# Kernel tuning notes

Hardware: AMD Instinct MI355X
Metric: run time of the kernel (lower is better)

## Reference

```python
import jax, jax.numpy as jnp
import numpy as np
from jax import lax

WIN = 7
K1 = 0.01
K2 = 0.03


def _box(t, w):
    # 'valid' box filter: uniform WINxWIN window, matches F.conv2d(t, w)
    return lax.conv_general_dilated(
        t, w, window_strides=(1, 1), padding='VALID',
        dimension_numbers=('NCHW', 'OIHW', 'NCHW'))


def setup_inputs() -> dict:
    key = jax.random.key(0)
    kx, ky = jax.random.split(key)
    X = jax.random.uniform(kx, (256, 1, 320, 320), dtype=jnp.float32)
    Y = jax.random.uniform(ky, (256, 1, 320, 320), dtype=jnp.float32)
    return {"X": X, "Y": Y}


def reference(X, Y):
    NP = WIN * WIN
    cov_norm = NP / (NP - 1)  # unbiased covariance correction
    w = jnp.ones((1, 1, WIN, WIN), X.dtype) / NP

    # per-sample dynamic range of the reference image Y -> [B,1,1,1]
    data_range = jnp.max(Y, axis=(1, 2, 3), keepdims=True)
    C1 = (K1 * data_range) ** 2
    C2 = (K2 * data_range) ** 2

    ux = _box(X, w)
    uy = _box(Y, w)
    uxx = _box(X * X, w)
    uyy = _box(Y * Y, w)
    uxy = _box(X * Y, w)

    vx = cov_norm * (uxx - ux * ux)
    vy = cov_norm * (uyy - uy * uy)
    vxy = cov_norm * (uxy - ux * uy)

    A1 = 2 * ux * uy + C1
    A2 = 2 * vxy + C2
    B1 = ux * ux + uy * uy + C1
    B2 = vx + vy + C2

    S = (A1 * A2) / (B1 * B2)
    S = jnp.mean(S)          # reduced=True
    return 1.0 - S           # as_loss=True
```

## Files before the change

### kernel.cpp

```cpp
#include <hip/hip_runtime.h>

#define BATCH 256
#define IMH 320
#define IMW 320
#define OUTD 314
#define WIN7 7
#define TOX 122
#define RCH 80

__global__ __launch_bounds__(256) void k_max(const float* __restrict__ Y,
                                             unsigned* __restrict__ dr) {
    int bid = blockIdx.x;
    int b = bid >> 2, part = bid & 3;
    const float4* p = (const float4*)(Y + (size_t)b * (IMH * IMW) + part * (IMH * IMW / 4));
    float m = 0.f;
    for (int i = threadIdx.x; i < (IMH * IMW / 16); i += 256) {
        float4 v = p[i];
        m = fmaxf(m, fmaxf(fmaxf(v.x, v.y), fmaxf(v.z, v.w)));
    }
    for (int off = 32; off; off >>= 1) m = fmaxf(m, __shfl_down(m, off, 64));
    __shared__ float sm[4];
    int lane = threadIdx.x & 63, wv = threadIdx.x >> 6;
    if (lane == 0) sm[wv] = m;
    __syncthreads();
    if (threadIdx.x == 0) {
        m = fmaxf(fmaxf(sm[0], sm[1]), fmaxf(sm[2], sm[3]));
        atomicMax(dr + b, __float_as_uint(m));
    }
}

__global__ __launch_bounds__(128) void k_ssim(const float* __restrict__ X,
                                              const float* __restrict__ Y,
                                              const unsigned* __restrict__ dr,
                                              double* __restrict__ acc) {
    int idx = blockIdx.x;
    int b = idx / 12;
    int rem = idx - b * 12;
    int ct = rem % 3;
    int rc = rem / 3;
    int t  = threadIdx.x;
    int c  = ct * TOX + t;
    int r0 = rc * RCH;
    int nout = min(RCH, OUTD - r0);
    bool colload = (c < IMW);

    const size_t base = (size_t)b * (IMH * IMW);
    const float* Xp = X + base;
    const float* Yp = Y + base;

    float drv = __uint_as_float(dr[b]);
    float c1r = 0.01f * drv, c2r = 0.03f * drv;
    float C1 = c1r * c1r;
    float C2 = c2r * c2r;

    __shared__ float vs[5][132];

    float x0=0,x1=0,x2=0,x3=0,x4=0,x5=0,x6=0;
    float y0=0,y1=0,y2=0,y3=0,y4=0,y5=0,y6=0;
    float sx=0, sy=0, sxx=0, syy=0, sxy=0;
    float part = 0.f;

    int rend = r0 + nout + (WIN7 - 2);
    for (int r = r0; r <= rend; ++r) {
        float xn = 0.f, yn = 0.f;
        if (colload) {
            xn = Xp[(size_t)r * IMW + c];
            yn = Yp[(size_t)r * IMW + c];
        }
        sx  += xn - x0;
        sy  += yn - y0;
        sxx += xn * xn - x0 * x0;
        syy += yn * yn - y0 * y0;
        sxy += xn * yn - x0 * y0;
        x0=x1; x1=x2; x2=x3; x3=x4; x4=x5; x5=x6; x6=xn;
        y0=y1; y1=y2; y2=y3; y3=y4; y4=y5; y5=y6; y6=yn;

        if (r - r0 >= WIN7 - 1) {
            vs[0][t]=sx; vs[1][t]=sy; vs[2][t]=sxx; vs[3][t]=syy; vs[4][t]=sxy;
            __syncthreads();
            int co = ct * TOX + t;
            if (t < TOX && co < OUTD) {
                float hsx=0, hsy=0, hsxx=0, hsyy=0, hsxy=0;
                #pragma unroll
                for (int d = 0; d < WIN7; ++d) {
                    hsx  += vs[0][t + d];
                    hsy  += vs[1][t + d];
                    hsxx += vs[2][t + d];
                    hsyy += vs[3][t + d];
                    hsxy += vs[4][t + d];
                }
                const float inv = 1.f / 49.f;
                const float cn  = 49.f / 48.f;
                float ux  = hsx  * inv, uy  = hsy  * inv;
                float uxx = hsxx * inv, uyy = hsyy * inv, uxy = hsxy * inv;
                float vx  = cn * (uxx - ux * ux);
                float vy  = cn * (uyy - uy * uy);
                float vxy = cn * (uxy - ux * uy);
                float A1 = 2.f * ux * uy + C1;
                float A2 = 2.f * vxy + C2;
                float B1 = ux * ux + uy * uy + C1;
                float B2 = vx + vy + C2;
                part += (A1 * A2) / (B1 * B2);
            }
            __syncthreads();
        }
    }

    for (int off = 32; off; off >>= 1) part += __shfl_down(part, off, 64);
    __shared__ float ps[2];
    if ((threadIdx.x & 63) == 0) ps[threadIdx.x >> 6] = part;
    __syncthreads();
    if (threadIdx.x == 0) atomicAdd(acc, (double)(ps[0] + ps[1]));
}

__global__ void k_final(const double* __restrict__ acc, float* __restrict__ out) {
    const double cnt = (double)BATCH * (double)OUTD * (double)OUTD;
    out[0] = (float)(1.0 - acc[0] / cnt);
}

extern "C" void kernel_launch(void* const* d_in, const int* in_sizes, int n_in,
                              void* d_out, int out_size, void* d_ws, size_t ws_size,
                              hipStream_t stream) {
    const float* X = (const float*)d_in[0];
    const float* Y = (const float*)d_in[1];
    float* out = (float*)d_out;

    unsigned* dr = (unsigned*)d_ws;
    double* acc  = (double*)((char*)d_ws + 1024);

    hipMemsetAsync(d_ws, 0, 2048, stream);
    k_max <<<BATCH * 4, 256, 0, stream>>>(Y, dr);
    k_ssim<<<BATCH * 12, 128, 0, stream>>>(X, Y, dr, acc);
    k_final<<<1, 1, 0, stream>>>(acc, out);
}
```

Baseline: 319.1 us.

## Rework SSIM kernel: full-row float2 columns, merged variance sums, double-buffered LDS

Each block now covers a full image row with 160 active threads, each owning two columns loaded as float2. This removes the column-tile halo overlap and the 3-way column split. The xx and yy sums are merged into one sum of squares, and the ring buffer is fully unrolled into registers. Double-buffered shared memory removes one barrier per row, horizontal sums are shared between the two output pixels, and the division is replaced with a fast reciprocal. Row chunks shrink to 36 outputs, so vertical halo rows are reloaded more often and the reciprocal loses a little precision.

```diff
diff --git a/kernel.cpp b/kernel.cpp
--- a/kernel.cpp
+++ b/kernel.cpp
@@ -4,9 +4,10 @@
 #define IMH 320
 #define IMW 320
 #define OUTD 314
-#define WIN7 7
-#define TOX 122
-#define RCH 80
+#define NCH 9
+#define RCH 36
+#define ITERS 42
+#define NTHR 192
 
 __global__ __launch_bounds__(256) void k_max(const float* __restrict__ Y,
                                              unsigned* __restrict__ dr) {
@@ -29,88 +30,96 @@
     }
 }
 
-__global__ __launch_bounds__(128) void k_ssim(const float* __restrict__ X,
-                                              const float* __restrict__ Y,
-                                              const unsigned* __restrict__ dr,
-                                              double* __restrict__ acc) {
-    int idx = blockIdx.x;
-    int b = idx / 12;
-    int rem = idx - b * 12;
-    int ct = rem % 3;
-    int rc = rem / 3;
-    int t  = threadIdx.x;
-    int c  = ct * TOX + t;
-    int r0 = rc * RCH;
-    int nout = min(RCH, OUTD - r0);
-    bool colload = (c < IMW);
+__device__ __forceinline__ float ssim_px(float hx, float hy, float hp, float hxy,
+                                         float C1, float C2) {
+    const float inv = 1.f / 49.f;
+    const float cn  = 49.f / 48.f;
+    float ux  = hx  * inv, uy = hy * inv;
+    float upp = hp  * inv;
+    float uxy = hxy * inv;
+    float ux2 = ux * ux, uy2 = uy * uy, uxuy = ux * uy;
+    float B2 = cn * (upp - ux2 - uy2) + C2;
+    float A2 = 2.f * cn * (uxy - uxuy) + C2;
+    float A1 = 2.f * uxuy + C1;
+    float B1 = ux2 + uy2 + C1;
+    return (A1 * A2) * __builtin_amdgcn_rcpf(B1 * B2);
+}
 
-    const size_t base = (size_t)b * (IMH * IMW);
-    const float* Xp = X + base;
-    const float* Yp = Y + base;
+__global__ __launch_bounds__(NTHR) void k_ssim(const float* __restrict__ X,
+                                               const float* __restrict__ Y,
+                                               const unsigned* __restrict__ dr,
+                                               double* __restrict__ acc) {
+    const int idx = blockIdx.x;
+    const int b  = idx / NCH;
+    const int rc = idx - b * NCH;
+    const int t  = threadIdx.x;
+    const int r0 = rc * RCH;
+    const int nout = min(RCH, OUTD - r0);
+    const bool act = (t < IMW / 2);
+    const bool rdr = (t <= (OUTD - 2) / 2);
 
-    float drv = __uint_as_float(dr[b]);
-    float c1r = 0.01f * drv, c2r = 0.03f * drv;
-    float C1 = c1r * c1r;
-    float C2 = c2r * c2r;
+    const float2* Xp = (const float2*)(X + (size_t)b * (IMH * IMW));
+    const float2* Yp = (const float2*)(Y + (size_t)b * (IMH * IMW));
 
-    __shared__ float vs[5][132];
+    const float drv = __uint_as_float(dr[b]);
+    const float c1s = 0.01f * drv, c2s = 0.03f * drv;
+    const float C1 = c1s * c1s, C2 = c2s * c2s;
 
-    float x0=0,x1=0,x2=0,x3=0,x4=0,x5=0,x6=0;
-    float y0=0,y1=0,y2=0,y3=0,y4=0,y5=0,y6=0;
-    float sx=0, sy=0, sxx=0, syy=0, sxy=0;
+    __shared__ float2 vs[2][4][NTHR + 4];
+
+    float2 rx[7], ry[7];
+    #pragma unroll
+    for (int k = 0; k < 7; ++k) { rx[k] = make_float2(0.f, 0.f); ry[k] = make_float2(0.f, 0.f); }
+    float2 sx  = make_float2(0.f, 0.f), sy  = make_float2(0.f, 0.f);
+    float2 sp  = make_float2(0.f, 0.f), sxy = make_float2(0.f, 0.f);
     float part = 0.f;
 
-    int rend = r0 + nout + (WIN7 - 2);
-    for (int r = r0; r <= rend; ++r) {
-        float xn = 0.f, yn = 0.f;
-        if (colload) {
-            xn = Xp[(size_t)r * IMW + c];
-            yn = Yp[(size_t)r * IMW + c];
-        }
-        sx  += xn - x0;
-        sy  += yn - y0;
-        sxx += xn * xn - x0 * x0;
-        syy += yn * yn - y0 * y0;
-        sxy += xn * yn - x0 * y0;
-        x0=x1; x1=x2; x2=x3; x3=x4; x4=x5; x5=x6; x6=xn;
-        y0=y1; y1=y2; y2=y3; y3=y4; y4=y5; y5=y6; y6=yn;
-
-        if (r - r0 >= WIN7 - 1) {
-            vs[0][t]=sx; vs[1][t]=sy; vs[2][t]=sxx; vs[3][t]=syy; vs[4][t]=sxy;
-            __syncthreads();
-            int co = ct * TOX + t;
-            if (t < TOX && co < OUTD) {
-                float hsx=0, hsy=0, hsxx=0, hsyy=0, hsxy=0;
-                #pragma unroll
-                for (int d = 0; d < WIN7; ++d) {
-                    hsx  += vs[0][t + d];
-                    hsy  += vs[1][t + d];
-                    hsxx += vs[2][t + d];
-                    hsyy += vs[3][t + d];
-                    hsxy += vs[4][t + d];
-                }
-                const float inv = 1.f / 49.f;
-                const float cn  = 49.f / 48.f;
-                float ux  = hsx  * inv, uy  = hsy  * inv;
-                float uxx = hsxx * inv, uyy = hsyy * inv, uxy = hsxy * inv;
-                float vx  = cn * (uxx - ux * ux);
-                float vy  = cn * (uyy - uy * uy);
-                float vxy = cn * (uxy - ux * uy);
-                float A1 = 2.f * ux * uy + C1;
-                float A2 = 2.f * vxy + C2;
-                float B1 = ux * ux + uy * uy + C1;
-                float B2 = vx + vy + C2;
-                part += (A1 * A2) / (B1 * B2);
-            }
-            __syncthreads();
-        }
+    #define VBODY(K, I7) {                                                     \
+        const int i = (I7) + (K);                                              \
+        const int r = r0 + i;                                                  \
+        float2 xn = make_float2(0.f, 0.f), yn = make_float2(0.f, 0.f);         \
+        if (act && r < IMH) { xn = Xp[r * (IMW/2) + t]; yn = Yp[r * (IMW/2) + t]; } \
+        const float2 ox = rx[K], oy = ry[K];                                   \
+        sx.x  += xn.x - ox.x;              sx.y  += xn.y - ox.y;               \
+        sy.x  += yn.x - oy.x;              sy.y  += yn.y - oy.y;               \
+        sp.x  += (xn.x*xn.x + yn.x*yn.x) - (ox.x*ox.x + oy.x*oy.x);            \
+        sp.y  += (xn.y*xn.y + yn.y*yn.y) - (ox.y*ox.y + oy.y*oy.y);            \
+        sxy.x += xn.x*yn.x - ox.x*oy.x;    sxy.y += xn.y*yn.y - ox.y*oy.y;     \
+        rx[K] = xn; ry[K] = yn;                                                \
+        if (i >= 6) {                                      \
+            const int par = i & 1;                                             \
+            if (act) { vs[par][0][t] = sx;  vs[par][1][t] = sy;                \
+                       vs[par][2][t] = sp;  vs[par][3][t] = sxy; }             \
+            __syncthreads();                                                   \
+            if (rdr && (i - 6 < nout)) {                                       \
+                float h0[4], h1[4];                                            \
+                _Pragma("unroll")                                              \
+                for (int q = 0; q < 4; ++q) {                                  \
+                    float2 v0 = vs[par][q][t],     v1 = vs[par][q][t + 1];     \
+                    float2 v2 = vs[par][q][t + 2], v3 = vs[par][q][t + 3];     \
+                    float s8 = ((v0.x + v0.y) + (v1.x + v1.y))                 \
+                             + ((v2.x + v2.y) + (v3.x + v3.y));                \
+                    h0[q] = s8 - v3.y;             \
+                    h1[q] = s8 - v0.x;             \
+                }                                                              \
+                part += ssim_px(h0[0], h0[1], h0[2], h0[3], C1, C2);           \
+                part += ssim_px(h1[0], h1[1], h1[2], h1[3], C1, C2);           \
+            }                                                                  \
+        }                                                                      \
     }
 
+    for (int i7 = 0; i7 < ITERS; i7 += 7) {
+        VBODY(0, i7) VBODY(1, i7) VBODY(2, i7) VBODY(3, i7)
+        VBODY(4, i7) VBODY(5, i7) VBODY(6, i7)
+    }
+    #undef VBODY
+
     for (int off = 32; off; off >>= 1) part += __shfl_down(part, off, 64);
-    __shared__ float ps[2];
-    if ((threadIdx.x & 63) == 0) ps[threadIdx.x >> 6] = part;
+    __shared__ float ps[3];
+    const int lane = t & 63, wv = t >> 6;
+    if (lane == 0) ps[wv] = part;
     __syncthreads();
-    if (threadIdx.x == 0) atomicAdd(acc, (double)(ps[0] + ps[1]));
+    if (t == 0) atomicAdd(acc, (double)((ps[0] + ps[1]) + ps[2]));
 }
 
 __global__ void k_final(const double* __restrict__ acc, float* __restrict__ out) {
@@ -130,6 +139,6 @@
 
     hipMemsetAsync(d_ws, 0, 2048, stream);
     k_max <<<BATCH * 4, 256, 0, stream>>>(Y, dr);
-    k_ssim<<<BATCH * 12, 128, 0, stream>>>(X, Y, dr, acc);
+    k_ssim<<<BATCH * NCH, NTHR, 0, stream>>>(X, Y, dr, acc);
     k_final<<<1, 1, 0, stream>>>(acc, out);
 }
```

Measured after the change: 281.3 us. 11.9% less time.
